# Optimization experiments

Measured on AMD Instinct MI355X. Metric: run time of the kernel, lower is better.

## Reference

```python
import jax, jax.numpy as jnp
import numpy as np

EPS = 1e-05


def _nearest_upsample(x, H, W):
    # torch F.interpolate default mode='nearest': src_idx = floor(dst_idx * in/out)
    h, w = x.shape[-2], x.shape[-1]
    rows = (jnp.arange(H) * h) // H
    cols = (jnp.arange(W) * w) // W
    return x[..., rows[:, None], cols[None, :]]


def _dilate(mask, k):
    # Grayscale dilation with a flat (all-ones) k x k structuring element ==
    # k x k max filter (kornia dilation w/ ones kernel). Geodesic border: pad -inf
    p = (k - 1) // 2
    return jax.lax.reduce_window(
        mask, -jnp.inf, jax.lax.max,
        window_dimensions=(1, 1, k, k),
        window_strides=(1, 1, 1, 1),
        padding=[(0, 0), (0, 0), (p, k - 1 - p), (p, k - 1 - p)],
    )


def setup_inputs() -> dict:
    key = jax.random.key(0)
    k1, k2 = jax.random.split(key)
    small = jax.random.normal(k1, (2, 4, 1, 270, 480), dtype=jnp.float32)
    large = jax.random.uniform(k2, (2, 4, 1, 1080, 1920), dtype=jnp.float32)
    return {"small": small, "large": large, "dilate_width": 7, "sigmoid": 1}


def reference(small, large, dilate_width, sigmoid):
    B, T = small.shape[0], small.shape[1]
    s = small.reshape((B * T,) + small.shape[2:])   # [BT, C, h, w]
    l = large.reshape((B * T,) + large.shape[2:])   # [BT, C, H, W]
    H, W = l.shape[-2], l.shape[-1]
    up = _nearest_upsample(s, H, W)
    t = jax.nn.sigmoid(up) if sigmoid else up
    trans = ((t > EPS) & (t < 1.0 - EPS)).astype(l.dtype)
    if dilate_width >= 1:
        trans = _dilate(trans, dilate_width)
    out = trans * l + (1.0 - trans) * up
    return out.reshape(large.shape)
```

## Files before the change

### kernel.cpp

```cpp
#include <hip/hip_runtime.h>
#include <cmath>

#define HS 270
#define WS 480
#define HL 1080
#define WL 1920

#define TILE_ROWS 8
#define TILE_GROUPS 32

__global__ __launch_bounds__(256) void PRM_77824807403842_kernel(
    const float* __restrict__ sml,
    const float* __restrict__ lrg,
    const int* __restrict__ sigp,
    float* __restrict__ out)
{
    const int bt = blockIdx.z;
    const int i0 = blockIdx.y * TILE_ROWS;
    const int p0 = blockIdx.x * TILE_GROUPS;
    const int q0 = i0 >> 2;
    const int tid = threadIdx.x;
    const int sig = *sigp;

    __shared__ unsigned int mword[TILE_GROUPS + 2];
    __shared__ float fval[2][TILE_GROUPS];

    const float* sb = sml + (size_t)bt * (HS * WS);

    if (tid < TILE_GROUPS + 2) {
        const int cc = p0 - 1 + tid;
        unsigned int w = 0;
        if (cc >= 0 && cc < WS) {
#pragma unroll
            for (int r = 0; r < 4; ++r) {
                const int rr = q0 - 1 + r;
                if (rr >= 0 && rr < HS) {
                    const float x = sb[(size_t)rr * WS + cc];
                    const float t = sig ? (1.0f / (1.0f + expf(-x))) : x;
                    const unsigned int m =
                        (t > 1e-5f && t < 0.99999f) ? 1u : 0u;
                    w |= m << (8 * r);
                }
            }
        }
        mword[tid] = w;
    } else if (tid >= 64 && tid < 64 + 2 * TILE_GROUPS) {
        const int idx = tid - 64;
        const int fr = idx >> 5;
        const int fc = idx & 31;
        fval[fr][fc] = sb[(size_t)(q0 + fr) * WS + (p0 + fc)];
    }
    __syncthreads();

    const int rl = tid >> 5;
    const int g  = tid & 31;
    const int i  = i0 + rl;
    const int q  = i >> 2;
    const int s  = i & 3;
    const int qi = q - q0;

    const unsigned int base =
        (s == 0) ? 0x0000FFFFu : ((s == 3) ? 0x00FFFF00u : 0x00FFFFFFu);
    const unsigned int sel = base << (8 * qi);

    const unsigned int wl_ = mword[g] & sel;
    const unsigned int wm_ = mword[g + 1] & sel;
    const unsigned int wr_ = mword[g + 2] & sel;

    const float up = fval[qi][g];

    const size_t off = ((size_t)bt * HL + i) * WL + 4 * (size_t)(p0 + g);
    const float4 l4 = *reinterpret_cast<const float4*>(lrg + off);

    const unsigned int all3 = wl_ | wm_ | wr_;
    float4 o;
    o.x = (wl_ | wm_) ? l4.x : up;
    o.y = all3        ? l4.y : up;
    o.z = all3        ? l4.z : up;
    o.w = (wm_ | wr_) ? l4.w : up;

    *reinterpret_cast<float4*>(out + off) = o;
}

extern "C" void kernel_launch(void* const* d_in, const int* in_sizes, int n_in,
                              void* d_out, int out_size, void* d_ws, size_t ws_size,
                              hipStream_t stream) {
    const float* sml = (const float*)d_in[0];
    const float* lrg = (const float*)d_in[1];
    const int* sigp = (const int*)d_in[3];
    float* outp = (float*)d_out;

    const int BT = in_sizes[1] / (HL * WL);

    dim3 grid(WL / (4 * TILE_GROUPS), HL / TILE_ROWS, BT);
    dim3 block(256);
    hipLaunchKernelGGL(PRM_77824807403842_kernel, grid, block, 0, stream,
                       sml, lrg, sigp, outp);
}
```

Baseline: 32.68 us.

## Widen tiles to 96 groups, prefetch large loads early, use nontemporal access

Each block now covers 96 column groups instead of 32, with each thread handling three float4s. The three large-tensor loads are issued before the shared-memory mask setup so their latency overlaps it. The center-row values are read once by the mask threads rather than reloaded separately. Large loads and output stores use nontemporal builtins to avoid cache pollution, and wider tiles cut per-block halo overhead and block count, at the cost of more registers per thread and fewer blocks for load balancing.

```diff
diff --git a/kernel.cpp b/kernel.cpp
--- a/kernel.cpp
+++ b/kernel.cpp
@@ -7,7 +7,10 @@
 #define WL 1920
 
 #define TILE_ROWS 8
-#define TILE_GROUPS 32
+#define GROUPS 96
+#define HALO (GROUPS + 2)
+
+typedef float f4 __attribute__((ext_vector_type(4)));
 
 __global__ __launch_bounds__(256) void PRM_77824807403842_kernel(
     const float* __restrict__ sml,
@@ -17,17 +20,27 @@
 {
     const int bt = blockIdx.z;
     const int i0 = blockIdx.y * TILE_ROWS;
-    const int p0 = blockIdx.x * TILE_GROUPS;
+    const int p0 = blockIdx.x * GROUPS;
     const int q0 = i0 >> 2;
     const int tid = threadIdx.x;
+
+    const int rl = tid >> 5;
+    const int g0 = tid & 31;
+    const int i  = i0 + rl;
+
+    const size_t rowoff = ((size_t)bt * HL + i) * WL + 4 * (size_t)p0;
+    const f4* lp = reinterpret_cast<const f4*>(lrg + rowoff);
+    const f4 l0 = __builtin_nontemporal_load(lp + g0);
+    const f4 l1 = __builtin_nontemporal_load(lp + g0 + 32);
+    const f4 l2 = __builtin_nontemporal_load(lp + g0 + 64);
+
+    __shared__ unsigned int mword[HALO];
+    __shared__ float fval[2][GROUPS];
+
+    const float* sb = sml + (size_t)bt * (HS * WS);
     const int sig = *sigp;
 
-    __shared__ unsigned int mword[TILE_GROUPS + 2];
-    __shared__ float fval[2][TILE_GROUPS];
-
-    const float* sb = sml + (size_t)bt * (HS * WS);
-
-    if (tid < TILE_GROUPS + 2) {
+    if (tid < HALO) {
         const int cc = p0 - 1 + tid;
         unsigned int w = 0;
         if (cc >= 0 && cc < WS) {
@@ -37,24 +50,16 @@
                 if (rr >= 0 && rr < HS) {
                     const float x = sb[(size_t)rr * WS + cc];
                     const float t = sig ? (1.0f / (1.0f + expf(-x))) : x;
-                    const unsigned int m =
-                        (t > 1e-5f && t < 0.99999f) ? 1u : 0u;
-                    w |= m << (8 * r);
+                    w |= ((t > 1e-5f && t < 0.99999f) ? 1u : 0u) << (8 * r);
+                    if ((r == 1 || r == 2) && tid >= 1 && tid <= GROUPS)
+                        fval[r - 1][tid - 1] = x;
                 }
             }
         }
         mword[tid] = w;
-    } else if (tid >= 64 && tid < 64 + 2 * TILE_GROUPS) {
-        const int idx = tid - 64;
-        const int fr = idx >> 5;
-        const int fc = idx & 31;
-        fval[fr][fc] = sb[(size_t)(q0 + fr) * WS + (p0 + fc)];
     }
     __syncthreads();
 
-    const int rl = tid >> 5;
-    const int g  = tid & 31;
-    const int i  = i0 + rl;
     const int q  = i >> 2;
     const int s  = i & 3;
     const int qi = q - q0;
@@ -63,23 +68,25 @@
         (s == 0) ? 0x0000FFFFu : ((s == 3) ? 0x00FFFF00u : 0x00FFFFFFu);
     const unsigned int sel = base << (8 * qi);
 
-    const unsigned int wl_ = mword[g] & sel;
-    const unsigned int wm_ = mword[g + 1] & sel;
-    const unsigned int wr_ = mword[g + 2] & sel;
+    f4* op = reinterpret_cast<f4*>(out + rowoff);
 
-    const float up = fval[qi][g];
+#pragma unroll
+    for (int k = 0; k < 3; ++k) {
+        const int g = g0 + 32 * k;
+        const unsigned int wl_ = mword[g]     & sel;
+        const unsigned int wm_ = mword[g + 1] & sel;
+        const unsigned int wr_ = mword[g + 2] & sel;
+        const float up = fval[qi][g];
+        const f4 l4 = (k == 0) ? l0 : (k == 1) ? l1 : l2;
 
-    const size_t off = ((size_t)bt * HL + i) * WL + 4 * (size_t)(p0 + g);
-    const float4 l4 = *reinterpret_cast<const float4*>(lrg + off);
-
-    const unsigned int all3 = wl_ | wm_ | wr_;
-    float4 o;
-    o.x = (wl_ | wm_) ? l4.x : up;
-    o.y = all3        ? l4.y : up;
-    o.z = all3        ? l4.z : up;
-    o.w = (wm_ | wr_) ? l4.w : up;
-
-    *reinterpret_cast<float4*>(out + off) = o;
+        const unsigned int all3 = wl_ | wm_ | wr_;
+        f4 o;
+        o.x = (wl_ | wm_) ? l4.x : up;
+        o.y = all3        ? l4.y : up;
+        o.z = all3        ? l4.z : up;
+        o.w = (wm_ | wr_) ? l4.w : up;
+        __builtin_nontemporal_store(o, op + g);
+    }
 }
 
 extern "C" void kernel_launch(void* const* d_in, const int* in_sizes, int n_in,
@@ -92,7 +99,7 @@
 
     const int BT = in_sizes[1] / (HL * WL);
 
-    dim3 grid(WL / (4 * TILE_GROUPS), HL / TILE_ROWS, BT);
+    dim3 grid(WL / (4 * GROUPS), HL / TILE_ROWS, BT);
     dim3 block(256);
     hipLaunchKernelGGL(PRM_77824807403842_kernel, grid, block, 0, stream,
                        sml, lrg, sigp, outp);
```

Result: faster. 28.43 us (-13.0%).

## Map one thread per small pixel, computing 4x4 output patch with nontemporal I/O

Applied to the files above, without the earlier changes.

Each thread now handles one low-res pixel and writes its full 4x4 high-res patch. It reads the 3x3 small neighbourhood directly from global memory, with no shared memory and no barrier. The sigmoid is replaced by equivalent logit thresholds, which removes the exp. Large-tensor loads and output stores use nontemporal hints. The trade-off is redundant neighbour reads per thread (served by cache) and a strided row access pattern across four rows.

```diff
diff --git a/kernel.cpp b/kernel.cpp
--- a/kernel.cpp
+++ b/kernel.cpp
@@ -6,8 +6,7 @@
 #define HL 1080
 #define WL 1920
 
-#define TILE_ROWS 8
-#define TILE_GROUPS 32
+typedef float f4 __attribute__((ext_vector_type(4)));
 
 __global__ __launch_bounds__(256) void PRM_77824807403842_kernel(
     const float* __restrict__ sml,
@@ -15,71 +14,61 @@
     const int* __restrict__ sigp,
     float* __restrict__ out)
 {
+    const int n = blockIdx.x * 256 + threadIdx.x;
+    if (n >= HS * WS) return;
     const int bt = blockIdx.z;
-    const int i0 = blockIdx.y * TILE_ROWS;
-    const int p0 = blockIdx.x * TILE_GROUPS;
-    const int q0 = i0 >> 2;
-    const int tid = threadIdx.x;
-    const int sig = *sigp;
+    const int q = n / WS;
+    const int P = n - q * WS;
 
-    __shared__ unsigned int mword[TILE_GROUPS + 2];
-    __shared__ float fval[2][TILE_GROUPS];
+    const size_t lbase = ((size_t)bt * HL + 4 * (size_t)q) * WL + 4 * (size_t)P;
+    const f4* lp = reinterpret_cast<const f4*>(lrg + lbase);
+    const f4 l0 = __builtin_nontemporal_load(lp + 0 * (WL / 4));
+    const f4 l1 = __builtin_nontemporal_load(lp + 1 * (WL / 4));
+    const f4 l2 = __builtin_nontemporal_load(lp + 2 * (WL / 4));
+    const f4 l3 = __builtin_nontemporal_load(lp + 3 * (WL / 4));
 
     const float* sb = sml + (size_t)bt * (HS * WS);
+    const int qm = q > 0 ? q - 1 : 0;
+    const int qp = q < HS - 1 ? q + 1 : q;
+    const int Pm = P > 0 ? P - 1 : 0;
+    const int Pp = P < WS - 1 ? P + 1 : P;
+    const unsigned vqm = q > 0, vqp = q < HS - 1;
+    const unsigned vPm = P > 0, vPp = P < WS - 1;
 
-    if (tid < TILE_GROUPS + 2) {
-        const int cc = p0 - 1 + tid;
-        unsigned int w = 0;
-        if (cc >= 0 && cc < WS) {
-#pragma unroll
-            for (int r = 0; r < 4; ++r) {
-                const int rr = q0 - 1 + r;
-                if (rr >= 0 && rr < HS) {
-                    const float x = sb[(size_t)rr * WS + cc];
-                    const float t = sig ? (1.0f / (1.0f + expf(-x))) : x;
-                    const unsigned int m =
-                        (t > 1e-5f && t < 0.99999f) ? 1u : 0u;
-                    w |= m << (8 * r);
-                }
-            }
-        }
-        mword[tid] = w;
-    } else if (tid >= 64 && tid < 64 + 2 * TILE_GROUPS) {
-        const int idx = tid - 64;
-        const int fr = idx >> 5;
-        const int fc = idx & 31;
-        fval[fr][fc] = sb[(size_t)(q0 + fr) * WS + (p0 + fc)];
-    }
-    __syncthreads();
+    const float x00 = sb[(size_t)qm * WS + Pm], x01 = sb[(size_t)qm * WS + P], x02 = sb[(size_t)qm * WS + Pp];
+    const float x10 = sb[(size_t)q  * WS + Pm], x11 = sb[(size_t)q  * WS + P], x12 = sb[(size_t)q  * WS + Pp];
+    const float x20 = sb[(size_t)qp * WS + Pm], x21 = sb[(size_t)qp * WS + P], x22 = sb[(size_t)qp * WS + Pp];
 
-    const int rl = tid >> 5;
-    const int g  = tid & 31;
-    const int i  = i0 + rl;
-    const int q  = i >> 2;
-    const int s  = i & 3;
-    const int qi = q - q0;
+    const int sig = *sigp;
+    auto msk = [&](float x) -> unsigned {
+        return sig ? (unsigned)((x > -11.5129154f) & (x < 11.5129054f))
+                   : (unsigned)((x > 1e-5f) & (x < 0.99999f));
+    };
 
-    const unsigned int base =
-        (s == 0) ? 0x0000FFFFu : ((s == 3) ? 0x00FFFF00u : 0x00FFFFFFu);
-    const unsigned int sel = base << (8 * qi);
+    const unsigned M00 = msk(x00) & vqm & vPm, M01 = msk(x01) & vqm, M02 = msk(x02) & vqm & vPp;
+    const unsigned M10 = msk(x10) & vPm,       M11 = msk(x11),       M12 = msk(x12) & vPp;
+    const unsigned M20 = msk(x20) & vqp & vPm, M21 = msk(x21) & vqp, M22 = msk(x22) & vqp & vPp;
 
-    const unsigned int wl_ = mword[g] & sel;
-    const unsigned int wm_ = mword[g + 1] & sel;
-    const unsigned int wr_ = mword[g + 2] & sel;
+    const unsigned r0c0 = M00 | M10, r0c1 = M01 | M11, r0c2 = M02 | M12;
+    const unsigned r2c0 = M10 | M20, r2c1 = M11 | M21, r2c2 = M12 | M22;
+    const unsigned r1c0 = r0c0 | M20, r1c1 = r0c1 | M21, r1c2 = r0c2 | M22;
 
-    const float up = fval[qi][g];
+    const float up = x11;
+    auto sel4 = [&](unsigned c0, unsigned c1, unsigned c2, f4 l) -> f4 {
+        const unsigned L = c0 | c1, A = L | c2, R = c1 | c2;
+        f4 o;
+        o.x = L ? l.x : up;
+        o.y = A ? l.y : up;
+        o.z = A ? l.z : up;
+        o.w = R ? l.w : up;
+        return o;
+    };
 
-    const size_t off = ((size_t)bt * HL + i) * WL + 4 * (size_t)(p0 + g);
-    const float4 l4 = *reinterpret_cast<const float4*>(lrg + off);
-
-    const unsigned int all3 = wl_ | wm_ | wr_;
-    float4 o;
-    o.x = (wl_ | wm_) ? l4.x : up;
-    o.y = all3        ? l4.y : up;
-    o.z = all3        ? l4.z : up;
-    o.w = (wm_ | wr_) ? l4.w : up;
-
-    *reinterpret_cast<float4*>(out + off) = o;
+    f4* op = reinterpret_cast<f4*>(out + lbase);
+    __builtin_nontemporal_store(sel4(r0c0, r0c1, r0c2, l0), op + 0 * (WL / 4));
+    __builtin_nontemporal_store(sel4(r1c0, r1c1, r1c2, l1), op + 1 * (WL / 4));
+    __builtin_nontemporal_store(sel4(r1c0, r1c1, r1c2, l2), op + 2 * (WL / 4));
+    __builtin_nontemporal_store(sel4(r2c0, r2c1, r2c2, l3), op + 3 * (WL / 4));
 }
 
 extern "C" void kernel_launch(void* const* d_in, const int* in_sizes, int n_in,
@@ -92,7 +81,7 @@
 
     const int BT = in_sizes[1] / (HL * WL);
 
-    dim3 grid(WL / (4 * TILE_GROUPS), HL / TILE_ROWS, BT);
+    dim3 grid((HS * WS + 255) / 256, 1, BT);
     dim3 block(256);
     hipLaunchKernelGGL(PRM_77824807403842_kernel, grid, block, 0, stream,
                        sml, lrg, sigp, outp);
```

After: 27.00 us (median of 3 runs). -17.4%, faster.
